# Performance work log

Measured on AMD Instinct MI355X. Metric: run time of the kernel, lower is better.

Reference implementation:

```python
import jax, jax.numpy as jnp
import numpy as np


def setup_inputs() -> dict:
    key = jax.random.key(0)
    k0, k1, k2, k3 = jax.random.split(key, 4)
    B, M, H, K, OUT = 256, 64, 64, 128, 256
    x0 = jax.random.normal(k0, (B, M, K), dtype=jnp.float32)
    xl = jax.random.normal(k1, (B, H, K), dtype=jnp.float32)
    # Conv1d(in_channels=M*H, out_channels=OUT, kernel_size=1) params
    fan_in = M * H  # kernel_size=1
    bound = 1.0 / np.sqrt(fan_in)
    W = jax.random.uniform(k2, (OUT, M * H, 1), dtype=jnp.float32, minval=-bound, maxval=bound)
    b = jax.random.uniform(k3, (OUT,), dtype=jnp.float32, minval=-bound, maxval=bound)
    return {"x0": x0, "xl": xl, "k": K, "W": W, "b": b}


def reference(x0, xl, k, W, b):
    # x0: [B, m, k_emb], xl: [B, h, k_emb]
    # Fused equivalent of the per-column loop: for each embedding column i,
    # matmul(xl[:,:,i:i+1], x0[:,:,i:i+1]^T) -> [B,h,m]; stacked over k -> [B,h,m,k]
    fmap = jnp.einsum('bhk,bmk->bhmk', xl, x0)
    B = x0.shape[0]
    h, m = xl.shape[1], x0.shape[1]
    fmap = fmap.reshape(B, h * m, k)  # [B, h*m, k]
    # 1x1 Conv1d == GEMM over channel dim
    out = jnp.einsum('bck,oc->bok', fmap, W[:, :, 0]) + b[None, :, None]
    return out
```

## Files before the change

### kernel.cpp

```cpp
#include <hip/hip_runtime.h>
#include <hip/hip_bf16.h>
#include <stdint.h>


typedef __attribute__((ext_vector_type(8)))  short short8;
typedef __attribute__((ext_vector_type(16))) float f32x16;

#define B_SZ   256
#define K_SZ   128
#define OUT_SZ 256
#define C_SZ   4096
#define NH     64

__device__ __forceinline__ uint32_t pack_bf16(float a, float b) {
    __hip_bfloat162 h2 = __float22bfloat162_rn(make_float2(a, b));
    union { __hip_bfloat162 h; uint32_t u; } v;
    v.h = h2;
    return v.u;
}

__device__ __forceinline__ float bf2f(short s) {
    union { uint32_t u; float f; } v;
    v.u = ((uint32_t)(uint16_t)s) << 16;
    return v.f;
}

__device__ __forceinline__ void load_lds_16(const void* g, void* l) {
    __builtin_amdgcn_global_load_lds(
        (const __attribute__((address_space(1))) unsigned int*)g,
        (__attribute__((address_space(3))) unsigned int*)l,
        16, 0, 0);
}

__global__ void convert_W_tiled(const float* __restrict__ W, short* __restrict__ Wb) {
    int t = blockIdx.x * blockDim.x + threadIdx.x;
    int lane = t & 63;
    int sub  = t >> 6;
    int cb16 = sub & 255;
    int got  = sub >> 8;
    int o = got * 32 + (lane & 31);
    int c = cb16 * 16 + (lane >> 5) * 8;
    const float* p = W + (size_t)o * C_SZ + c;
    float4 w0 = *(const float4*)p;
    float4 w1 = *(const float4*)(p + 4);
    union { short8 s; uint32_t u[4]; } cc;
    cc.u[0] = pack_bf16(w0.x, w0.y);
    cc.u[1] = pack_bf16(w0.z, w0.w);
    cc.u[2] = pack_bf16(w1.x, w1.y);
    cc.u[3] = pack_bf16(w1.z, w1.w);
    *(short8*)(Wb + (size_t)t * 8) = cc.s;
}

template<bool USE_WS>
__global__ __launch_bounds__(256, 2)
void cin_main(const float* __restrict__ x0, const float* __restrict__ xl,
              const float* __restrict__ Wf, const short* __restrict__ Wb,
              const float* __restrict__ bias, float* __restrict__ out) {
    __shared__ short Wlds[4 * 3 * 2048];
    __shared__ short xls[NH * K_SZ];

    const int b     = blockIdx.y;
    const int ohalf = blockIdx.x;
    const int tid   = threadIdx.x;
    const int lane  = tid & 63;
    const int wave  = tid >> 6;
    const int got   = ohalf * 4 + wave;
    const int l31   = lane & 31;
    const int hi    = lane >> 5;

    {
        const float4* src = (const float4*)(xl + (size_t)b * (NH * K_SZ));
        uint32_t* dst = (uint32_t*)&xls[tid * 32];
#pragma unroll
        for (int i = 0; i < 8; ++i) {
            float4 v = src[tid * 8 + i];
            dst[2 * i]     = pack_bf16(v.x, v.y);
            dst[2 * i + 1] = pack_bf16(v.z, v.w);
        }
    }

    union { short8 s; uint32_t u[4]; } x0p[4][4];
    {
        const float* x0b = x0 + (size_t)b * (64 * K_SZ);
#pragma unroll
        for (int s = 0; s < 4; ++s)
#pragma unroll
            for (int nt = 0; nt < 4; ++nt)
#pragma unroll
                for (int t2 = 0; t2 < 4; ++t2) {
                    const int m0 = s * 16 + hi * 8 + 2 * t2;
                    const int cc = nt * 32 + l31;
                    x0p[s][nt].u[t2] = pack_bf16(x0b[m0 * K_SZ + cc],
                                                 x0b[(m0 + 1) * K_SZ + cc]);
                }
    }

    const short* wsrc  = Wb + ((size_t)got * 256) * 512 + lane * 8;
    const float* wfrow = Wf + (size_t)(got * 32 + l31) * C_SZ + hi * 8;
    short* wl = Wlds + wave * (3 * 2048);

    auto stage = [&](int buf, int h) {
        if (USE_WS) {
            const short* s0 = wsrc + (size_t)(4 * h) * 512;
            short* d = wl + buf * 2048;
#pragma unroll
            for (int sub = 0; sub < 4; ++sub)
                load_lds_16(s0 + sub * 512, d + sub * 512);
        } else {
#pragma unroll
            for (int sub = 0; sub < 4; ++sub) {
                const float* p = wfrow + h * 64 + sub * 16;
                float4 w0 = *(const float4*)p;
                float4 w1 = *(const float4*)(p + 4);
                union { short8 s; uint32_t u[4]; } cc;
                cc.u[0] = pack_bf16(w0.x, w0.y);
                cc.u[1] = pack_bf16(w0.z, w0.w);
                cc.u[2] = pack_bf16(w1.x, w1.y);
                cc.u[3] = pack_bf16(w1.z, w1.w);
                *(short8*)(wl + buf * 2048 + sub * 512 + lane * 8) = cc.s;
            }
        }
    };

    f32x16 acc[4];
#pragma unroll
    for (int nt = 0; nt < 4; ++nt)
#pragma unroll
        for (int r = 0; r < 16; ++r) acc[nt][r] = 0.f;
    f32x16 kz;
#pragma unroll
    for (int r = 0; r < 16; ++r) kz[r] = 0.f;

    stage(0, 0);
    stage(1, 1);
    __syncthreads();

    int buf = 0;
    for (int h = 0; h < NH; ++h) {
        if (USE_WS) asm volatile("s_waitcnt vmcnt(4)" ::: "memory");

        int bn = buf + 2; if (bn >= 3) bn -= 3;
        stage(bn, (h + 2) & (NH - 1));

        const short* wb2 = wl + buf * 2048 + lane * 8;
        const short8 af0 = *(const short8*)(wb2);
        const short8 af1 = *(const short8*)(wb2 + 512);
        const short8 af2 = *(const short8*)(wb2 + 1024);
        const short8 af3 = *(const short8*)(wb2 + 1536);

        float xlv[4];
#pragma unroll
        for (int nt = 0; nt < 4; ++nt)
            xlv[nt] = bf2f(xls[h * K_SZ + nt * 32 + l31]);

#pragma unroll
        for (int nt = 0; nt < 4; ++nt) {
            f32x16 g = __builtin_amdgcn_mfma_f32_32x32x16_bf16(af0, x0p[0][nt].s, kz, 0, 0, 0);
            g = __builtin_amdgcn_mfma_f32_32x32x16_bf16(af1, x0p[1][nt].s, g, 0, 0, 0);
            g = __builtin_amdgcn_mfma_f32_32x32x16_bf16(af2, x0p[2][nt].s, g, 0, 0, 0);
            g = __builtin_amdgcn_mfma_f32_32x32x16_bf16(af3, x0p[3][nt].s, g, 0, 0, 0);
#pragma unroll
            for (int r = 0; r < 16; ++r)
                acc[nt][r] += xlv[nt] * g[r];
        }

        buf += 1; if (buf == 3) buf = 0;
    }

    float bv[16];
#pragma unroll
    for (int r = 0; r < 16; ++r)
        bv[r] = bias[got * 32 + (r & 3) + 8 * (r >> 2) + 4 * hi];

    float* outb = out + (size_t)b * (OUT_SZ * K_SZ);
#pragma unroll
    for (int nt = 0; nt < 4; ++nt) {
        const int kcol = nt * 32 + l31;
#pragma unroll
        for (int r = 0; r < 16; ++r) {
            const int orow = got * 32 + (r & 3) + 8 * (r >> 2) + 4 * hi;
            outb[orow * K_SZ + kcol] = acc[nt][r] + bv[r];
        }
    }
}

extern "C" void kernel_launch(void* const* d_in, const int* in_sizes, int n_in,
                              void* d_out, int out_size, void* d_ws, size_t ws_size,
                              hipStream_t stream) {
    const float* x0   = (const float*)d_in[0];
    const float* xl   = (const float*)d_in[1];
    const float* W    = (const float*)d_in[3];
    const float* bias = (const float*)d_in[4];
    float* out = (float*)d_out;

    const size_t w_bytes = (size_t)OUT_SZ * C_SZ * sizeof(short);
    short* Wb = (short*)d_ws;

    if (ws_size >= w_bytes) {
        convert_W_tiled<<<dim3(512), dim3(256), 0, stream>>>(W, Wb);
        cin_main<true><<<dim3(2, B_SZ), dim3(256), 0, stream>>>(x0, xl, W, Wb, bias, out);
    } else {
        cin_main<false><<<dim3(2, B_SZ), dim3(256), 0, stream>>>(x0, xl, W, Wb, bias, out);
    }
}
```

Measured before the change: 79.16 us.

## Software-pipeline MFMA chains with deferred accumulation and double-buffered W staging

Reorders the main loop so the scalar FMA accumulation of each MFMA chain result is deferred and interleaved with the next MFMA chain, using two alternating temporaries and carrying the last two tails into the next iteration. Wave priority is raised around the MFMA block. The W LDS ring shrinks from triple to double buffering, and staging now happens after the fragment reads, guarded by an lgkmcnt wait. This aims to hide MFMA result latency behind VALU work and to cut LDS use, at the cost of less prefetch distance for the async global-to-LDS loads.

```diff
diff --git a/kernel.cpp b/kernel.cpp
--- a/kernel.cpp
+++ b/kernel.cpp
@@ -56,7 +56,7 @@
 void cin_main(const float* __restrict__ x0, const float* __restrict__ xl,
               const float* __restrict__ Wf, const short* __restrict__ Wb,
               const float* __restrict__ bias, float* __restrict__ out) {
-    __shared__ short Wlds[4 * 3 * 2048];
+    __shared__ short Wlds[4 * 2 * 2048];
     __shared__ short xls[NH * K_SZ];
 
     const int b     = blockIdx.y;
@@ -97,7 +97,7 @@
 
     const short* wsrc  = Wb + ((size_t)got * 256) * 512 + lane * 8;
     const float* wfrow = Wf + (size_t)(got * 32 + l31) * C_SZ + hi * 8;
-    short* wl = Wlds + wave * (3 * 2048);
+    short* wl = Wlds + wave * (2 * 2048);
 
     auto stage = [&](int buf, int h) {
         if (USE_WS) {
@@ -135,37 +135,59 @@
     stage(1, 1);
     __syncthreads();
 
-    int buf = 0;
+    f32x16 gE = kz, gO = kz;
+    float px2 = 0.f, px3 = 0.f;
+
+#define CHAIN(G, NT)                                                                   \
+    do {                                                                               \
+        G = __builtin_amdgcn_mfma_f32_32x32x16_bf16(af0, x0p[0][NT].s, kz, 0, 0, 0);   \
+        G = __builtin_amdgcn_mfma_f32_32x32x16_bf16(af1, x0p[1][NT].s, G, 0, 0, 0);    \
+        G = __builtin_amdgcn_mfma_f32_32x32x16_bf16(af2, x0p[2][NT].s, G, 0, 0, 0);    \
+        G = __builtin_amdgcn_mfma_f32_32x32x16_bf16(af3, x0p[3][NT].s, G, 0, 0, 0);    \
+    } while (0)
+
+#define TAIL(ACC_I, PX, G)                                                             \
+    do {                                                                               \
+        _Pragma("unroll")                                                              \
+        for (int r = 0; r < 16; ++r) acc[ACC_I][r] += (PX) * G[r];                     \
+    } while (0)
+
     for (int h = 0; h < NH; ++h) {
         if (USE_WS) asm volatile("s_waitcnt vmcnt(4)" ::: "memory");
 
-        int bn = buf + 2; if (bn >= 3) bn -= 3;
-        stage(bn, (h + 2) & (NH - 1));
-
-        const short* wb2 = wl + buf * 2048 + lane * 8;
+        const short* wb2 = wl + (h & 1) * 2048 + lane * 8;
         const short8 af0 = *(const short8*)(wb2);
         const short8 af1 = *(const short8*)(wb2 + 512);
         const short8 af2 = *(const short8*)(wb2 + 1024);
         const short8 af3 = *(const short8*)(wb2 + 1536);
 
-        float xlv[4];
-#pragma unroll
-        for (int nt = 0; nt < 4; ++nt)
-            xlv[nt] = bf2f(xls[h * K_SZ + nt * 32 + l31]);
-
-#pragma unroll
-        for (int nt = 0; nt < 4; ++nt) {
-            f32x16 g = __builtin_amdgcn_mfma_f32_32x32x16_bf16(af0, x0p[0][nt].s, kz, 0, 0, 0);
-            g = __builtin_amdgcn_mfma_f32_32x32x16_bf16(af1, x0p[1][nt].s, g, 0, 0, 0);
-            g = __builtin_amdgcn_mfma_f32_32x32x16_bf16(af2, x0p[2][nt].s, g, 0, 0, 0);
-            g = __builtin_amdgcn_mfma_f32_32x32x16_bf16(af3, x0p[3][nt].s, g, 0, 0, 0);
-#pragma unroll
-            for (int r = 0; r < 16; ++r)
-                acc[nt][r] += xlv[nt] * g[r];
-        }
-
-        buf += 1; if (buf == 3) buf = 0;
-    }
+        const float xlv0 = bf2f(xls[h * K_SZ + 0 * 32 + l31]);
+        const float xlv1 = bf2f(xls[h * K_SZ + 1 * 32 + l31]);
+        const float xlv2 = bf2f(xls[h * K_SZ + 2 * 32 + l31]);
+        const float xlv3 = bf2f(xls[h * K_SZ + 3 * 32 + l31]);
+
+        __builtin_amdgcn_s_setprio(1);
+        TAIL(2, px2, gE);
+        CHAIN(gE, 0);
+        TAIL(3, px3, gO);
+        CHAIN(gO, 1);
+        TAIL(0, xlv0, gE);
+        CHAIN(gE, 2);
+        TAIL(1, xlv1, gO);
+        CHAIN(gO, 3);
+        __builtin_amdgcn_s_setprio(0);
+
+        px2 = xlv2;
+        px3 = xlv3;
+
+        asm volatile("s_waitcnt lgkmcnt(0)" ::: "memory");
+        stage(h & 1, (h + 2) & (NH - 1));
+    }
+
+    TAIL(2, px2, gE);
+    TAIL(3, px3, gO);
+#undef CHAIN
+#undef TAIL
 
     float bv[16];
 #pragma unroll
```

Measured after the change: 81.71 us. 1.03x slower.

## Fold xl scaling into MFMA B operand and split blocks over k

Applied to the files above, without the earlier changes.

Instead of computing a per-h partial GEMM into a temporary and scaling it by xl with VALU FMAs, the kernel scales x0 by xl on the fly when packing the bf16 B operand, so MFMAs accumulate straight into the output accumulators. Blocks are now split over halves of the k dimension, not the output dimension, with each wave handling two 32-row output tiles. W staging moves to double-buffered LDS with a wait and restage after compute. The change aims to remove the 64 VALU FMAs per tile per h and the zero-init MFMA chains. In exchange it adds per-h bf16 packing of scaled x0 and keeps x0 in fp32 registers, which raises register pressure. Rounding also changes because the product is now rounded to bf16.

```diff
diff --git a/kernel.cpp b/kernel.cpp
--- a/kernel.cpp
+++ b/kernel.cpp
@@ -17,12 +17,6 @@
     union { __hip_bfloat162 h; uint32_t u; } v;
     v.h = h2;
     return v.u;
-}
-
-__device__ __forceinline__ float bf2f(short s) {
-    union { uint32_t u; float f; } v;
-    v.u = ((uint32_t)(uint16_t)s) << 16;
-    return v.f;
 }
 
 __device__ __forceinline__ void load_lds_16(const void* g, void* l) {
@@ -56,130 +50,133 @@
 void cin_main(const float* __restrict__ x0, const float* __restrict__ xl,
               const float* __restrict__ Wf, const short* __restrict__ Wb,
               const float* __restrict__ bias, float* __restrict__ out) {
-    __shared__ short Wlds[4 * 3 * 2048];
-    __shared__ short xls[NH * K_SZ];
+    __shared__ short Wlds[2 * 4 * 4096];
+    __shared__ float xlf[NH * 64];
 
     const int b     = blockIdx.y;
-    const int ohalf = blockIdx.x;
+    const int khalf = blockIdx.x;
+    const int kb    = khalf * 64;
     const int tid   = threadIdx.x;
     const int lane  = tid & 63;
     const int wave  = tid >> 6;
-    const int got   = ohalf * 4 + wave;
     const int l31   = lane & 31;
     const int hi    = lane >> 5;
 
     {
-        const float4* src = (const float4*)(xl + (size_t)b * (NH * K_SZ));
-        uint32_t* dst = (uint32_t*)&xls[tid * 32];
-#pragma unroll
-        for (int i = 0; i < 8; ++i) {
-            float4 v = src[tid * 8 + i];
-            dst[2 * i]     = pack_bf16(v.x, v.y);
-            dst[2 * i + 1] = pack_bf16(v.z, v.w);
-        }
-    }
-
-    union { short8 s; uint32_t u[4]; } x0p[4][4];
+        const float4* src = (const float4*)(xl + (size_t)b * (NH * K_SZ)
+                                            + (tid >> 2) * K_SZ + kb + (tid & 3) * 16);
+        float4* dst = (float4*)&xlf[(tid >> 2) * 64 + (tid & 3) * 16];
+#pragma unroll
+        for (int i = 0; i < 4; ++i) dst[i] = src[i];
+    }
+
+    float x0f[4][2][8];
     {
         const float* x0b = x0 + (size_t)b * (64 * K_SZ);
 #pragma unroll
-        for (int s = 0; s < 4; ++s)
-#pragma unroll
-            for (int nt = 0; nt < 4; ++nt)
-#pragma unroll
-                for (int t2 = 0; t2 < 4; ++t2) {
-                    const int m0 = s * 16 + hi * 8 + 2 * t2;
-                    const int cc = nt * 32 + l31;
-                    x0p[s][nt].u[t2] = pack_bf16(x0b[m0 * K_SZ + cc],
-                                                 x0b[(m0 + 1) * K_SZ + cc]);
+        for (int cb = 0; cb < 4; ++cb)
+#pragma unroll
+            for (int nt = 0; nt < 2; ++nt)
+#pragma unroll
+                for (int j = 0; j < 8; ++j)
+                    x0f[cb][nt][j] = x0b[(cb * 16 + hi * 8 + j) * K_SZ + kb + nt * 32 + l31];
+    }
+
+    const short* wsrc0 = Wb + ((size_t)(2 * wave) * 256) * 512 + lane * 8;
+    const short* wsrc1 = Wb + ((size_t)(2 * wave + 1) * 256) * 512 + lane * 8;
+    const float* wfrow0 = Wf + (size_t)(2 * wave * 32 + l31) * C_SZ + hi * 8;
+    const float* wfrow1 = wfrow0 + (size_t)32 * C_SZ;
+
+    auto wlb = [&](int buf) { return Wlds + buf * 16384 + wave * 4096; };
+
+    auto stage = [&](int buf, int h) {
+        short* d = wlb(buf);
+        if (USE_WS) {
+            const short* s0 = wsrc0 + (size_t)(4 * h) * 512;
+            const short* s1 = wsrc1 + (size_t)(4 * h) * 512;
+#pragma unroll
+            for (int cb = 0; cb < 4; ++cb)
+                load_lds_16(s0 + cb * 512, d + cb * 512);
+#pragma unroll
+            for (int cb = 0; cb < 4; ++cb)
+                load_lds_16(s1 + cb * 512, d + 2048 + cb * 512);
+        } else {
+#pragma unroll
+            for (int ot = 0; ot < 2; ++ot) {
+                const float* wf = ot ? wfrow1 : wfrow0;
+#pragma unroll
+                for (int cb = 0; cb < 4; ++cb) {
+                    const float* p = wf + h * 64 + cb * 16;
+                    float4 w0 = *(const float4*)p;
+                    float4 w1 = *(const float4*)(p + 4);
+                    union { short8 s; uint32_t u[4]; } cc;
+                    cc.u[0] = pack_bf16(w0.x, w0.y);
+                    cc.u[1] = pack_bf16(w0.z, w0.w);
+                    cc.u[2] = pack_bf16(w1.x, w1.y);
+                    cc.u[3] = pack_bf16(w1.z, w1.w);
+                    *(short8*)(d + ot * 2048 + cb * 512 + lane * 8) = cc.s;
                 }
-    }
-
-    const short* wsrc  = Wb + ((size_t)got * 256) * 512 + lane * 8;
-    const float* wfrow = Wf + (size_t)(got * 32 + l31) * C_SZ + hi * 8;
-    short* wl = Wlds + wave * (3 * 2048);
-
-    auto stage = [&](int buf, int h) {
-        if (USE_WS) {
-            const short* s0 = wsrc + (size_t)(4 * h) * 512;
-            short* d = wl + buf * 2048;
-#pragma unroll
-            for (int sub = 0; sub < 4; ++sub)
-                load_lds_16(s0 + sub * 512, d + sub * 512);
-        } else {
-#pragma unroll
-            for (int sub = 0; sub < 4; ++sub) {
-                const float* p = wfrow + h * 64 + sub * 16;
-                float4 w0 = *(const float4*)p;
-                float4 w1 = *(const float4*)(p + 4);
-                union { short8 s; uint32_t u[4]; } cc;
-                cc.u[0] = pack_bf16(w0.x, w0.y);
-                cc.u[1] = pack_bf16(w0.z, w0.w);
-                cc.u[2] = pack_bf16(w1.x, w1.y);
-                cc.u[3] = pack_bf16(w1.z, w1.w);
-                *(short8*)(wl + buf * 2048 + sub * 512 + lane * 8) = cc.s;
             }
         }
     };
 
-    f32x16 acc[4];
-#pragma unroll
-    for (int nt = 0; nt < 4; ++nt)
-#pragma unroll
-        for (int r = 0; r < 16; ++r) acc[nt][r] = 0.f;
-    f32x16 kz;
-#pragma unroll
-    for (int r = 0; r < 16; ++r) kz[r] = 0.f;
+    f32x16 acc[2][2];
+#pragma unroll
+    for (int ot = 0; ot < 2; ++ot)
+#pragma unroll
+        for (int nt = 0; nt < 2; ++nt)
+#pragma unroll
+            for (int r = 0; r < 16; ++r) acc[ot][nt][r] = 0.f;
 
     stage(0, 0);
     stage(1, 1);
     __syncthreads();
 
-    int buf = 0;
     for (int h = 0; h < NH; ++h) {
-        if (USE_WS) asm volatile("s_waitcnt vmcnt(4)" ::: "memory");
-
-        int bn = buf + 2; if (bn >= 3) bn -= 3;
-        stage(bn, (h + 2) & (NH - 1));
-
-        const short* wb2 = wl + buf * 2048 + lane * 8;
-        const short8 af0 = *(const short8*)(wb2);
-        const short8 af1 = *(const short8*)(wb2 + 512);
-        const short8 af2 = *(const short8*)(wb2 + 1024);
-        const short8 af3 = *(const short8*)(wb2 + 1536);
-
-        float xlv[4];
-#pragma unroll
-        for (int nt = 0; nt < 4; ++nt)
-            xlv[nt] = bf2f(xls[h * K_SZ + nt * 32 + l31]);
-
-#pragma unroll
-        for (int nt = 0; nt < 4; ++nt) {
-            f32x16 g = __builtin_amdgcn_mfma_f32_32x32x16_bf16(af0, x0p[0][nt].s, kz, 0, 0, 0);
-            g = __builtin_amdgcn_mfma_f32_32x32x16_bf16(af1, x0p[1][nt].s, g, 0, 0, 0);
-            g = __builtin_amdgcn_mfma_f32_32x32x16_bf16(af2, x0p[2][nt].s, g, 0, 0, 0);
-            g = __builtin_amdgcn_mfma_f32_32x32x16_bf16(af3, x0p[3][nt].s, g, 0, 0, 0);
-#pragma unroll
-            for (int r = 0; r < 16; ++r)
-                acc[nt][r] += xlv[nt] * g[r];
+        if (USE_WS) asm volatile("s_waitcnt vmcnt(8)" ::: "memory");
+
+        const short* wb2 = wlb(h & 1) + lane * 8;
+        short8 af[2][4];
+#pragma unroll
+        for (int ot = 0; ot < 2; ++ot)
+#pragma unroll
+            for (int cb = 0; cb < 4; ++cb)
+                af[ot][cb] = *(const short8*)(wb2 + ot * 2048 + cb * 512);
+
+        const float xlv0 = xlf[h * 64 + 0 * 32 + l31];
+        const float xlv1 = xlf[h * 64 + 1 * 32 + l31];
+
+        __builtin_amdgcn_s_setprio(1);
+#pragma unroll
+        for (int cb = 0; cb < 4; ++cb) {
+            union { short8 s; uint32_t u[4]; } b0, b1;
+#pragma unroll
+            for (int t2 = 0; t2 < 4; ++t2) {
+                b0.u[t2] = pack_bf16(xlv0 * x0f[cb][0][2 * t2], xlv0 * x0f[cb][0][2 * t2 + 1]);
+                b1.u[t2] = pack_bf16(xlv1 * x0f[cb][1][2 * t2], xlv1 * x0f[cb][1][2 * t2 + 1]);
+            }
+            acc[0][0] = __builtin_amdgcn_mfma_f32_32x32x16_bf16(af[0][cb], b0.s, acc[0][0], 0, 0, 0);
+            acc[0][1] = __builtin_amdgcn_mfma_f32_32x32x16_bf16(af[0][cb], b1.s, acc[0][1], 0, 0, 0);
+            acc[1][0] = __builtin_amdgcn_mfma_f32_32x32x16_bf16(af[1][cb], b0.s, acc[1][0], 0, 0, 0);
+            acc[1][1] = __builtin_amdgcn_mfma_f32_32x32x16_bf16(af[1][cb], b1.s, acc[1][1], 0, 0, 0);
         }
-
-        buf += 1; if (buf == 3) buf = 0;
-    }
-
-    float bv[16];
-#pragma unroll
-    for (int r = 0; r < 16; ++r)
-        bv[r] = bias[got * 32 + (r & 3) + 8 * (r >> 2) + 4 * hi];
+        __builtin_amdgcn_s_setprio(0);
+
+        asm volatile("s_waitcnt lgkmcnt(0)" ::: "memory");
+        stage(h & 1, (h + 2) & (NH - 1));
+    }
 
     float* outb = out + (size_t)b * (OUT_SZ * K_SZ);
 #pragma unroll
-    for (int nt = 0; nt < 4; ++nt) {
-        const int kcol = nt * 32 + l31;
+    for (int ot = 0; ot < 2; ++ot) {
+        const int obase = (2 * wave + ot) * 32;
 #pragma unroll
         for (int r = 0; r < 16; ++r) {
-            const int orow = got * 32 + (r & 3) + 8 * (r >> 2) + 4 * hi;
-            outb[orow * K_SZ + kcol] = acc[nt][r] + bv[r];
+            const int orow = obase + (r & 3) + 8 * (r >> 2) + 4 * hi;
+            const float bv = bias[orow];
+#pragma unroll
+            for (int nt = 0; nt < 2; ++nt)
+                outb[orow * K_SZ + kb + nt * 32 + l31] = acc[ot][nt][r] + bv;
         }
     }
 }
```

New measurement: 98.57 us. 24.5% more time.
